# Kernel tuning notes

Measured on AMD Instinct MI355X. Metric: run time of the kernel, lower is better.

## Reference

```python
import jax, jax.numpy as jnp
import numpy as np

N, H, T, E, L = 10000, 512, 4, 40000, 2
TIMESTEPS = (2, 2)  # layer_timesteps


def setup_inputs() -> dict:
    key = jax.random.key(0)
    ks = jax.random.split(key, 10)
    s = 1.0 / np.sqrt(H)
    u = lambda k, shape: jax.random.uniform(k, shape, jnp.float32, -s, s)
    return {
        "x": jax.random.normal(ks[0], (N, H), jnp.float32),
        "edges": jax.random.randint(ks[1], (T, E, 2), 0, N),  # (src, tgt)
        "W_msg": u(ks[2], (L, T, H, H)),   # torch Linear weight [out, in]
        "b_msg": u(ks[3], (L, T, H)),
        "W_ih": u(ks[4], (L, 3 * H, H)),   # GRUCell input weights (r,z,n)
        "W_hh": u(ks[5], (L, 3 * H, H)),
        "b_ih": u(ks[6], (L, 3 * H)),
        "b_hh": u(ks[7], (L, 3 * H)),
        "fc_W": u(ks[8], (H, H)),
        "fc_b": u(ks[9], (H,)),
    }


def _gru_cell(x, h, W_ih, W_hh, b_ih, b_hh):
    # torch.nn.GRUCell math
    gi = x @ W_ih.T + b_ih  # [N, 3H]
    gh = h @ W_hh.T + b_hh
    i_r, i_z, i_n = jnp.split(gi, 3, axis=-1)
    h_r, h_z, h_n = jnp.split(gh, 3, axis=-1)
    r = jax.nn.sigmoid(i_r + h_r)
    z = jax.nn.sigmoid(i_z + h_z)
    n = jnp.tanh(i_n + r * h_n)
    return (1.0 - z) * n + z * h


def reference(x, edges, W_msg, b_msg, W_ih, W_hh, b_ih, b_hh, fc_W, fc_b):
    # dropout layers run in eval mode (identity)
    targets = edges[:, :, 1].reshape(-1)  # [T*E], concat order matches torch loop
    sources = edges[:, :, 0]              # [T, E]
    h = x
    for layer in range(L):
        for _ in range(TIMESTEPS[layer]):
            src_states = h[sources]  # [T, E, H] gather
            # per-edge-type Linear: y = x @ W.T + b
            msgs = jnp.einsum('teh,tkh->tek', src_states, W_msg[layer]) \
                   + b_msg[layer][:, None, :]
            incoming = jax.ops.segment_sum(msgs.reshape(-1, H), targets,
                                           num_segments=N)  # scatter_add
            h = _gru_cell(incoming, h, W_ih[layer], W_hh[layer],
                          b_ih[layer], b_hh[layer])
    out = h @ fc_W.T + fc_b          # [N, H]
    graph_repr = jnp.max(out, axis=0)  # max-pool over nodes -> [H]
    return graph_repr
```

## Files before the change

### kernel.cpp

```cpp
#include <hip/hip_runtime.h>
#include <hip/hip_bf16.h>


#define NN 10000
#define HD 512
#define NT 4
#define NE 40000
#define CAP 24
#define GYROWS 80

typedef __bf16 bf16x8 __attribute__((ext_vector_type(8)));
typedef float f32x4 __attribute__((ext_vector_type(4)));
union V16 { int4 i; bf16x8 b; };

typedef __attribute__((address_space(1))) const unsigned int gu32;
typedef __attribute__((address_space(3))) unsigned int lu32;
__device__ __forceinline__ void gll16(const void* g, void* l) {
    __builtin_amdgcn_global_load_lds((gu32*)g, (lu32*)l, 16, 0, 0);
}

__device__ __forceinline__ float bfl(__bf16 v) { return (float)v; }

__device__ __forceinline__ int4 cvt8(const float* __restrict__ s) {
    float4 v0 = *(const float4*)s, v1 = *(const float4*)(s + 4);
    V16 o;
    o.b[0] = (__bf16)v0.x; o.b[1] = (__bf16)v0.y; o.b[2] = (__bf16)v0.z; o.b[3] = (__bf16)v0.w;
    o.b[4] = (__bf16)v1.x; o.b[5] = (__bf16)v1.y; o.b[6] = (__bf16)v1.z; o.b[7] = (__bf16)v1.w;
    return o.i;
}

__device__ __forceinline__ void pk_decode(int rem, int KTbits, int& col, int& kk) {
    int ct = rem >> (KTbits + 9);
    int r2 = rem & ((1 << (KTbits + 9)) - 1);
    int kt = r2 >> 9, s = r2 & 511;
    int lane = s & 63;
    col = ct * 128 + ((s >> 8) << 6) + (((s >> 6) & 3) << 4) + (lane & 15);
    kk = kt * 32 + ((lane >> 4) & 3) * 8;
}

__global__ void prep_all(const float* __restrict__ Wmsg, const float* __restrict__ Wih,
                         const float* __restrict__ Whh, const float* __restrict__ fcW,
                         const float* __restrict__ x, const int* __restrict__ edges,
                         int4* __restrict__ WmPK, int4* __restrict__ WrznhPK,
                         int4* __restrict__ WfPK,
                         float* __restrict__ h32, __hip_bfloat16* __restrict__ ab,
                         int* __restrict__ bcnt, int* __restrict__ bins) {
    int blk = blockIdx.x, tid = threadIdx.x;
    if (blk < 1024) {
        int g = blk * 256 + tid;
        int l = g >> 17, rem = g & 131071;
        int col, kk; pk_decode(rem, 4, col, kk);
        WmPK[g] = cvt8(Wmsg + (size_t)l * 1048576 + (size_t)col * 512 + kk);
        return;
    }
    blk -= 1024;
    if (blk < 2048) {
        int g = blk * 256 + tid;
        int l = g >> 18, rem = g & 262143;
        int col, kk; pk_decode(rem, 5, col, kk);
        int gate = (col >> 4) & 3;
        int hcol = ((col >> 7) * 2 + ((col >> 6) & 1)) * 16 + (col & 15);
        int4 v = make_int4(0, 0, 0, 0);
        if (kk < 512) {
            if (gate < 3) v = cvt8(Wih + (size_t)l * 786432 + (size_t)(gate * 512 + hcol) * 512 + kk);
        } else {
            if (gate < 2) v = cvt8(Whh + (size_t)l * 786432 + (size_t)(gate * 512 + hcol) * 512 + (kk - 512));
            else if (gate == 3) v = cvt8(Whh + (size_t)l * 786432 + (size_t)(1024 + hcol) * 512 + (kk - 512));
        }
        WrznhPK[g] = v;
        return;
    }
    blk -= 2048;
    if (blk < 128) {
        int g = blk * 256 + tid;
        int col, kk; pk_decode(g, 4, col, kk);
        WfPK[g] = cvt8(fcW + (size_t)col * 512 + kk);
        return;
    }
    blk -= 128;
    if (blk < 5000) {
        int i = blk * 1024 + tid * 4;
        float4 v = *(const float4*)(x + i);
        *(float4*)(h32 + i) = v;
        int m = i >> 9, c = i & 511;
        __hip_bfloat16 o[4] = {__float2bfloat16(v.x), __float2bfloat16(v.y),
                               __float2bfloat16(v.z), __float2bfloat16(v.w)};
        *(ulong1*)(ab + (size_t)m * 1024 + 512 + c) = *(ulong1*)o;
        return;
    }
    blk -= 5000;
    {
        int i = blk * 256 + tid;
        if (i >= NT * NE) return;
        int src = edges[2 * i], tgt = edges[2 * i + 1];
        int t = i / NE;
        int b = tgt * NT + t;
        int pos = atomicAdd(&bcnt[b], 1);
        if (pos < CAP) bins[(size_t)b * CAP + pos] = src;
    }
}

__global__ __launch_bounds__(256) void gather_msum(
    const int* __restrict__ bins, const int* __restrict__ bcnt,
    const float* __restrict__ bm, const __hip_bfloat16* __restrict__ Msg,
    __hip_bfloat16* __restrict__ inc) {
    int wave = threadIdx.x >> 6, lane = threadIdx.x & 63;
    int n = blockIdx.x * 4 + wave;
    int co = lane * 8;
    float acc[8] = {0, 0, 0, 0, 0, 0, 0, 0};
#pragma unroll
    for (int t = 0; t < NT; ++t) {
        int bi = n * NT + t;
        int cnt = bcnt[bi]; if (cnt > CAP) cnt = CAP;
        const int* bl = bins + (size_t)bi * CAP;
        for (int e = 0; e < cnt; ++e) {
            int src = bl[e];
            V16 v; v.i = *(const int4*)(Msg + (size_t)src * 2048 + t * 512 + co);
#pragma unroll
            for (int k = 0; k < 8; ++k) acc[k] += (float)v.b[k];
        }
        float4 b0 = *(const float4*)(bm + t * 512 + co);
        float4 b1 = *(const float4*)(bm + t * 512 + co + 4);
        float fc = (float)cnt;
        acc[0] += fc * b0.x; acc[1] += fc * b0.y; acc[2] += fc * b0.z; acc[3] += fc * b0.w;
        acc[4] += fc * b1.x; acc[5] += fc * b1.y; acc[6] += fc * b1.z; acc[7] += fc * b1.w;
    }
    V16 o;
#pragma unroll
    for (int k = 0; k < 8; ++k) o.b[k] = (__bf16)acc[k];
    *(int4*)(inc + (size_t)n * 1024 + co) = o.i;
}

__device__ __forceinline__ unsigned fenc(float f) {
    unsigned b = __float_as_uint(f);
    return b ^ (((int)b >> 31) | 0x80000000u);
}
__device__ __forceinline__ float fdec(unsigned u) {
    unsigned b = (u & 0x80000000u) ? (u ^ 0x80000000u) : ~u;
    return __uint_as_float(b);
}

template<int MODE>
__global__ __launch_bounds__(256) void gemm(
    const __hip_bfloat16* __restrict__ A, int lda, int K,
    const int4* __restrict__ Wpk,
    const float* __restrict__ b0, const float* __restrict__ b1,
    __hip_bfloat16* __restrict__ obf, int ldo,
    float* __restrict__ h32, unsigned* __restrict__ om) {
    __shared__ int4 sA4[3][1024];
    __shared__ unsigned sm[128];
    __hip_bfloat16* lds = (__hip_bfloat16*)sA4;
    float* ldsF = (float*)sA4;

    const int NB = (MODE == 3) ? 4 : 16;
    int bid = blockIdx.x;
    int xcd = bid & 7, kq = bid >> 3;
    int bcol = kq % NB;
    int brow = xcd + 8 * (kq / NB);
    int m0 = brow * 128, n0 = bcol * 128;

    int tid = threadIdx.x;
    int lane = tid & 63, wave = tid >> 6;
    int wr = wave >> 1, wc = wave & 1;
    int lm = lane & 15, quad = lane >> 4;
    int qx = (lm >> 1) & 3;

    const int KT32 = K >> 5;
    const int KT = K >> 6;
    const int kend = KT;
    const int4* Wp = Wpk + ((size_t)bcol * KT32 << 9) + wc * 256 + lane;

    auto issueA = [&](int kt, int p) {
        int k0 = kt << 6;
#pragma unroll
        for (int it = 0; it < 4; ++it) {
            int idx = it * 256 + tid;
            int s = idx >> 9, rem = idx & 511;
            int row = rem >> 2;
            int kc = (rem & 3) ^ ((row >> 1) & 3);
            int gm = m0 + row; gm = gm < NN ? gm : NN - 1;
            gll16(A + (size_t)gm * lda + k0 + s * 32 + kc * 8,
                  (__hip_bfloat16*)(sA4[p]) + idx * 8);
        }
    };
    auto loadB = [&](int kt, int4 (&bb)[2][4]) {
#pragma unroll
        for (int s = 0; s < 2; ++s) {
            const int4* wn = Wp + ((size_t)(2 * kt + s) << 9);
#pragma unroll
            for (int j = 0; j < 4; ++j) bb[s][j] = wn[j * 64];
        }
    };

    f32x4 acc[4][4] = {};
    int4 bb0[2][4], bb1[2][4];
    issueA(0, 0);
    issueA(1, 1);
    loadB(0, bb0);

    auto ktbody = [&](int kt, int4 (&bbCur)[2][4], int4 (&bbNxt)[2][4]) {
        int p = kt % 3;
        if (kt + 1 < kend) loadB(kt + 1, bbNxt);
        if (kt + 2 < kend) issueA(kt + 2, (kt + 2) % 3);
        __builtin_amdgcn_sched_barrier(0);
        if (kt + 2 < kend)      __builtin_amdgcn_s_waitcnt(0x4F78);
        else if (kt + 1 < kend) __builtin_amdgcn_s_waitcnt(0x4F74);
        else                    __builtin_amdgcn_s_waitcnt(0x0F78);
        __builtin_amdgcn_s_barrier();
        __builtin_amdgcn_sched_barrier(0);
        V16 a[4][2];
#pragma unroll
        for (int i = 0; i < 4; ++i)
#pragma unroll
            for (int s = 0; s < 2; ++s)
                a[i][s].i = sA4[p][s * 512 + (wr * 64 + i * 16 + lm) * 4 + (quad ^ qx)];
#pragma unroll
        for (int s = 0; s < 2; ++s)
#pragma unroll
            for (int i = 0; i < 4; ++i)
#pragma unroll
                for (int j = 0; j < 4; ++j) {
                    if (MODE == 1) {
                        if (j == 2 && kt >= 8) continue;
                        if (j == 3 && kt < 8) continue;
                    }
                    V16 b; b.i = bbCur[s][j];
                    acc[i][j] = __builtin_amdgcn_mfma_f32_16x16x32_bf16(a[i][s].b, b.b, acc[i][j], 0, 0, 0);
                }
        __builtin_amdgcn_sched_barrier(0);
        __builtin_amdgcn_s_barrier();
    };

    for (int k2 = 0; k2 < kend; k2 += 2) {
        ktbody(k2, bb0, bb1);
        ktbody(k2 + 1, bb1, bb0);
    }

    if (MODE == 0) {
#pragma unroll
        for (int ph = 0; ph < 2; ++ph) {
            if (wr == ph) {
#pragma unroll
                for (int j = 0; j < 4; ++j) {
                    int c = wc * 64 + j * 16 + lm;
#pragma unroll
                    for (int i = 0; i < 4; ++i)
#pragma unroll
                        for (int r = 0; r < 4; ++r)
                            lds[(i * 16 + quad * 4 + r) * 128 + c] = __float2bfloat16(acc[i][j][r]);
                }
            }
            __syncthreads();
#pragma unroll
            for (int q = 0; q < 4; ++q) {
                int idx = q * 256 + tid;
                int rl = idx >> 4, c16 = idx & 15;
                int m = m0 + ph * 64 + rl;
                if (m < NN)
                    *(int4*)(obf + (size_t)m * ldo + n0 + c16 * 8) =
                        *(const int4*)(lds + rl * 128 + c16 * 8);
            }
            __syncthreads();
        }
    } else if (MODE == 1) {
        int c32 = wc * 16 + lm;
        int hcol = bcol * 32 + c32;
        float rb = b0[hcol] + b1[hcol];
        float zb = b0[512 + hcol] + b1[512 + hcol];
        float ib = b0[1024 + hcol];
        float hb = b1[1024 + hcol];
#pragma unroll
        for (int i = 0; i < 4; ++i)
#pragma unroll
            for (int r = 0; r < 4; ++r) {
                int rloc = wr * 64 + i * 16 + quad * 4 + r;
                int m = m0 + rloc;
                float hp = 0.f;
                if (m < NN) hp = h32[(size_t)m * 512 + hcol];
                float rr = 1.f / (1.f + __expf(-(acc[i][0][r] + rb)));
                float zz = 1.f / (1.f + __expf(-(acc[i][1][r] + zb)));
                float nx = (acc[i][2][r] + ib) + rr * (acc[i][3][r] + hb);
                float n = 1.f - 2.f / (__expf(2.f * nx) + 1.f);
                ldsF[rloc * 33 + c32] = (1.f - zz) * n + zz * hp;
            }
        __syncthreads();
#pragma unroll
        for (int q = 0; q < 4; ++q) {
            int idx = q * 256 + tid;
            int rl = idx >> 3, c4 = (idx & 7) * 4;
            int m = m0 + rl;
            if (m < NN) {
                const float* pf = ldsF + rl * 33 + c4;
                float4 v = make_float4(pf[0], pf[1], pf[2], pf[3]);
                *(float4*)(h32 + (size_t)m * 512 + bcol * 32 + c4) = v;
                __hip_bfloat16 ob[4] = {__float2bfloat16(v.x), __float2bfloat16(v.y),
                                        __float2bfloat16(v.z), __float2bfloat16(v.w)};
                *(ulong1*)(obf + (size_t)m * ldo + bcol * 32 + c4) = *(ulong1*)ob;
            }
        }
    } else {
        if (tid < 128) sm[tid] = 0;
        __syncthreads();
#pragma unroll
        for (int j = 0; j < 4; ++j) {
            int c = wc * 64 + j * 16 + lm;
            float bias = b0[n0 + c];
            float mx = -INFINITY;
#pragma unroll
            for (int i = 0; i < 4; ++i) {
                int r0 = m0 + wr * 64 + i * 16 + quad * 4;
#pragma unroll
                for (int r = 0; r < 4; ++r) {
                    int m = r0 + r;
                    if (m < NN) mx = fmaxf(mx, acc[i][j][r] + bias);
                }
            }
            atomicMax(&sm[c], fenc(mx));
        }
        __syncthreads();
        if (tid < 128) atomicMax(&om[n0 + tid], sm[tid]);
    }
}

__global__ void writeout(const unsigned* __restrict__ om, float* __restrict__ o) {
    int c = threadIdx.x;
    o[c] = fdec(om[c]);
}

extern "C" void kernel_launch(void* const* d_in, const int* in_sizes, int n_in,
                              void* d_out, int out_size, void* d_ws, size_t ws_size,
                              hipStream_t stream) {
    (void)in_sizes; (void)n_in; (void)out_size; (void)ws_size;
    const float* x    = (const float*)d_in[0];
    const int*   edges= (const int*)d_in[1];
    const float* Wmsg = (const float*)d_in[2];
    const float* bmsg = (const float*)d_in[3];
    const float* Wih  = (const float*)d_in[4];
    const float* Whh  = (const float*)d_in[5];
    const float* bih  = (const float*)d_in[6];
    const float* bhh  = (const float*)d_in[7];
    const float* fcW  = (const float*)d_in[8];
    const float* fcb  = (const float*)d_in[9];
    float* out = (float*)d_out;

    char* ws = (char*)d_ws;
    size_t off = 0;
    auto alloc = [&](size_t bytes) -> void* {
        void* p = ws + off; off += (bytes + 255) & ~(size_t)255; return p;
    };
    float*          h32  = (float*)alloc((size_t)NN * HD * 4);
    __hip_bfloat16* abA  = (__hip_bfloat16*)alloc((size_t)NN * 1024 * 2);
    __hip_bfloat16* abB  = (__hip_bfloat16*)alloc((size_t)NN * 1024 * 2);
    int*            bcnt = (int*)alloc((size_t)NN * NT * 4);
    int*            bins = (int*)alloc((size_t)NN * NT * CAP * 4);
    unsigned*       om   = (unsigned*)alloc(HD * 4);
    int4*           WmPK   = (int4*)alloc((size_t)2 * 131072 * 16);
    int4*           WrznhPK= (int4*)alloc((size_t)2 * 262144 * 16);
    int4*           WfPK   = (int4*)alloc((size_t)32768 * 16);
    __hip_bfloat16* Msg  = (__hip_bfloat16*)alloc((size_t)NN * 2048 * 2);

    hipMemsetAsync(bcnt, 0, (size_t)NN * NT * 4, stream);
    hipMemsetAsync(om, 0, HD * 4, stream);
    prep_all<<<1024 + 2048 + 128 + 5000 + 625, 256, 0, stream>>>(
        Wmsg, Wih, Whh, fcW, x, edges, WmPK, WrznhPK, WfPK, h32, abA, bcnt, bins);

    for (int s = 0; s < 4; ++s) {
        int layer = s >> 1;
        __hip_bfloat16* cur = (s & 1) ? abB : abA;
        __hip_bfloat16* nxt = (s & 1) ? abA : abB;
        const int4* Wm = WmPK + (size_t)layer * 131072;
        const int4* Wz = WrznhPK + (size_t)layer * 262144;
        const float* bm = bmsg + (size_t)layer * 2048;
        const float* bi = bih + (size_t)layer * 1536;
        const float* bh = bhh + (size_t)layer * 1536;

        gemm<0><<<16 * GYROWS, 256, 0, stream>>>(cur + 512, 1024, 512, Wm,
            nullptr, nullptr, Msg, 2048, nullptr, nullptr);
        gather_msum<<<NN / 4, 256, 0, stream>>>(bins, bcnt, bm, Msg, cur);
        gemm<1><<<16 * GYROWS, 256, 0, stream>>>(cur, 1024, 1024, Wz,
            bi, bh, nxt + 512, 1024, h32, nullptr);
    }
    gemm<3><<<4 * GYROWS, 256, 0, stream>>>(abA + 512, 1024, 512, WfPK,
        fcb, nullptr, nullptr, 0, nullptr, om);
    writeout<<<1, 512, 0, stream>>>(om, out);
}
```

Before: 643.1 us.

## Load GEMM A tiles directly into registers instead of staging through LDS

Replaces the triple-buffered global_load_lds staging of the A operand with direct per-lane global loads into registers, double-buffered alongside the B fragments. This removes the LDS round trip and the per-k-step workgroup barriers, and shrinks shared memory so two blocks can fit per CU (launch_bounds 256,2). The cost is that each row of A is now fetched separately by the two column waves rather than shared through LDS. It also adds register pressure, and the 16-byte per-lane loads may be less coalesced.

```diff
diff --git a/kernel.cpp b/kernel.cpp
--- a/kernel.cpp
+++ b/kernel.cpp
@@ -12,12 +12,6 @@
 typedef __bf16 bf16x8 __attribute__((ext_vector_type(8)));
 typedef float f32x4 __attribute__((ext_vector_type(4)));
 union V16 { int4 i; bf16x8 b; };
-
-typedef __attribute__((address_space(1))) const unsigned int gu32;
-typedef __attribute__((address_space(3))) unsigned int lu32;
-__device__ __forceinline__ void gll16(const void* g, void* l) {
-    __builtin_amdgcn_global_load_lds((gu32*)g, (lu32*)l, 16, 0, 0);
-}
 
 __device__ __forceinline__ float bfl(__bf16 v) { return (float)v; }
 
@@ -141,16 +135,15 @@
 }
 
 template<int MODE>
-__global__ __launch_bounds__(256) void gemm(
+__global__ __launch_bounds__(256, 2) void gemm(
     const __hip_bfloat16* __restrict__ A, int lda, int K,
     const int4* __restrict__ Wpk,
     const float* __restrict__ b0, const float* __restrict__ b1,
     __hip_bfloat16* __restrict__ obf, int ldo,
     float* __restrict__ h32, unsigned* __restrict__ om) {
-    __shared__ int4 sA4[3][1024];
+    __shared__ float ldsF[128 * 33];
     __shared__ unsigned sm[128];
-    __hip_bfloat16* lds = (__hip_bfloat16*)sA4;
-    float* ldsF = (float*)sA4;
+    __hip_bfloat16* lds = (__hip_bfloat16*)ldsF;
 
     const int NB = (MODE == 3) ? 4 : 16;
     int bid = blockIdx.x;
@@ -163,25 +156,27 @@
     int lane = tid & 63, wave = tid >> 6;
     int wr = wave >> 1, wc = wave & 1;
     int lm = lane & 15, quad = lane >> 4;
-    int qx = (lm >> 1) & 3;
 
     const int KT32 = K >> 5;
     const int KT = K >> 6;
     const int kend = KT;
     const int4* Wp = Wpk + ((size_t)bcol * KT32 << 9) + wc * 256 + lane;
 
-    auto issueA = [&](int kt, int p) {
+    const __hip_bfloat16* Ar[4];
+#pragma unroll
+    for (int i = 0; i < 4; ++i) {
+        int gm = m0 + wr * 64 + i * 16 + lm;
+        gm = gm < NN ? gm : NN - 1;
+        Ar[i] = A + (size_t)gm * lda + quad * 8;
+    }
+
+    auto loadA = [&](int kt, V16 (&aa)[4][2]) {
         int k0 = kt << 6;
 #pragma unroll
-        for (int it = 0; it < 4; ++it) {
-            int idx = it * 256 + tid;
-            int s = idx >> 9, rem = idx & 511;
-            int row = rem >> 2;
-            int kc = (rem & 3) ^ ((row >> 1) & 3);
-            int gm = m0 + row; gm = gm < NN ? gm : NN - 1;
-            gll16(A + (size_t)gm * lda + k0 + s * 32 + kc * 8,
-                  (__hip_bfloat16*)(sA4[p]) + idx * 8);
-        }
+        for (int i = 0; i < 4; ++i)
+#pragma unroll
+            for (int s = 0; s < 2; ++s)
+                aa[i][s].i = *(const int4*)(Ar[i] + k0 + s * 32);
     };
     auto loadB = [&](int kt, int4 (&bb)[2][4]) {
 #pragma unroll
@@ -193,27 +188,18 @@
     };
 
     f32x4 acc[4][4] = {};
-    int4 bb0[2][4], bb1[2][4];
-    issueA(0, 0);
-    issueA(1, 1);
-    loadB(0, bb0);
-
-    auto ktbody = [&](int kt, int4 (&bbCur)[2][4], int4 (&bbNxt)[2][4]) {
-        int p = kt % 3;
-        if (kt + 1 < kend) loadB(kt + 1, bbNxt);
-        if (kt + 2 < kend) issueA(kt + 2, (kt + 2) % 3);
+    V16 a0[4][2], a1[4][2];
+    int4 br0[2][4], br1[2][4];
+    loadA(0, a0);
+    loadB(0, br0);
+
+    auto ktbody = [&](int kt, V16 (&aC)[4][2], V16 (&aN)[4][2],
+                      int4 (&bC)[2][4], int4 (&bN)[2][4]) {
+        if (kt + 1 < kend) { loadA(kt + 1, aN); loadB(kt + 1, bN); }
         __builtin_amdgcn_sched_barrier(0);
-        if (kt + 2 < kend)      __builtin_amdgcn_s_waitcnt(0x4F78);
-        else if (kt + 1 < kend) __builtin_amdgcn_s_waitcnt(0x4F74);
-        else                    __builtin_amdgcn_s_waitcnt(0x0F78);
-        __builtin_amdgcn_s_barrier();
+        if (kt + 1 < kend) __builtin_amdgcn_s_waitcnt(0x4F70);
+        else               __builtin_amdgcn_s_waitcnt(0x0F70);
         __builtin_amdgcn_sched_barrier(0);
-        V16 a[4][2];
-#pragma unroll
-        for (int i = 0; i < 4; ++i)
-#pragma unroll
-            for (int s = 0; s < 2; ++s)
-                a[i][s].i = sA4[p][s * 512 + (wr * 64 + i * 16 + lm) * 4 + (quad ^ qx)];
 #pragma unroll
         for (int s = 0; s < 2; ++s)
 #pragma unroll
@@ -224,16 +210,14 @@
                         if (j == 2 && kt >= 8) continue;
                         if (j == 3 && kt < 8) continue;
                     }
-                    V16 b; b.i = bbCur[s][j];
-                    acc[i][j] = __builtin_amdgcn_mfma_f32_16x16x32_bf16(a[i][s].b, b.b, acc[i][j], 0, 0, 0);
+                    V16 b; b.i = bC[s][j];
+                    acc[i][j] = __builtin_amdgcn_mfma_f32_16x16x32_bf16(aC[i][s].b, b.b, acc[i][j], 0, 0, 0);
                 }
-        __builtin_amdgcn_sched_barrier(0);
-        __builtin_amdgcn_s_barrier();
     };
 
     for (int k2 = 0; k2 < kend; k2 += 2) {
-        ktbody(k2, bb0, bb1);
-        ktbody(k2 + 1, bb1, bb0);
+        ktbody(k2, a0, a1, br0, br1);
+        ktbody(k2 + 1, a1, a0, br1, br0);
     }
 
     if (MODE == 0) {
```

Measured after the change: 871.1 us. 35.5% more time.
